# Kernel tuning notes

Measured on AMD Instinct MI355X. Metric: run time of the kernel, lower is better.

Reference implementation:

```python
import jax, jax.numpy as jnp
import numpy as np

GRID = 256  # hardcoded mask shape in the original module
SMOOTH = 1e-06
THRESH = 127.0


def _fill_polygon(pts):
    # pts: [N,1,2] in [0,1]; replicates the TF scan-line rasterizer, vectorized.
    p = jnp.clip(jnp.squeeze(pts, axis=1) * 255.0, 0.0, 255.0)  # [N,2]
    pj = jnp.roll(p, 1, axis=0)                                  # edge partner j=i-1 (wraps)
    y = jnp.arange(GRID, dtype=p.dtype)[:, None]                 # [R,1] scanline rows
    pi_y = p[None, :, 1]
    pj_y = pj[None, :, 1]
    # edge crosses scanline y (strict-below / at-or-above parity rule)
    cross = ((pi_y < y) & (pj_y >= y)) | ((pj_y < y) & (pi_y >= y))  # [R,N]
    denom = jnp.where(cross, pj_y - pi_y, 1.0)
    xint = p[None, :, 0] + (y - pi_y) / denom * (pj[None, :, 0] - p[None, :, 0])
    xs = jnp.sort(jnp.where(cross, xint, jnp.inf), axis=1)       # [R,N] valid xs first
    count = jnp.sum(cross, axis=1)                               # [R]
    starts = jnp.floor(xs[:, 0::2])                              # int cast of nonneg = floor
    ends = jnp.floor(xs[:, 1::2])                                # [R,P]
    pidx = jnp.arange(starts.shape[1])
    valid = (2 * pidx + 1)[None, :] < count[:, None]             # unpaired last node dropped
    xg = jnp.arange(GRID, dtype=p.dtype)
    span = ((xg[None, :, None] >= starts[:, None, :]) &
            (xg[None, :, None] <= ends[:, None, :]) &
            valid[:, None, :])                                   # [R,256,P]
    return jnp.any(span, axis=2).astype(jnp.float32)             # [256,256]


def _dice(y_true, y_pred):
    t = y_true.reshape(-1)
    q = y_pred.reshape(-1)
    inter = jnp.sum(t * q)
    return (2.0 * inter + SMOOTH) / (jnp.sum(t) + jnp.sum(q) + SMOOTH)


def setup_inputs() -> dict:
    key = jax.random.key(0)
    k1, k2 = jax.random.split(key)
    points = jax.random.uniform(k1, (64, 128, 1, 2), dtype=jnp.float32)
    dmap = jax.random.uniform(k2, (64, 256, 256, 1), dtype=jnp.float32)
    return {"points": points, "dmap": dmap}


def reference(points, dmap):
    masks = jax.vmap(_fill_polygon)(points)                       # [B,256,256]
    bin_mask = (dmap[..., 0] * 255.0 <= THRESH).astype(jnp.float32)  # [B,256,256]
    dices = jax.vmap(_dice)(masks, bin_mask)                      # [B]
    return jnp.mean(1.0 - dices)
```

## Files before the change

kernel.cpp:

```cpp
#include <hip/hip_runtime.h>

#define GRIDN  256
#define NPTS   128
#define NBATCH 64

__device__ __forceinline__ float2 scale_clip(float2 p) {
    return make_float2(fminf(fmaxf(p.x * 255.0f, 0.0f), 255.0f),
                       fminf(fmaxf(p.y * 255.0f, 0.0f), 255.0f));
}

__device__ __forceinline__ int covered(int A, int B) {
    const int hi = (A - 1) & ~1;
    const int lo = (B - 1) > 0 ? (B - 1) : 0;
    return (A > 0) && (hi >= lo);
}

__global__ __launch_bounds__(256) void fill_dice_kernel(
    const float* __restrict__ points,
    const float* __restrict__ dmap,
    unsigned int* __restrict__ acc)
{
#pragma clang fp contract(off)
    __shared__ unsigned int hist[4][GRIDN];
    __shared__ int psum[4][3];

    const int wave = threadIdx.x >> 6;
    const int lane = threadIdx.x & 63;
    const int blk  = blockIdx.x;
    const int b    = blk >> 6;
    const int y    = (blk & 63) * 4 + wave;
    const float yf = (float)y;

    *(uint4*)&hist[wave][lane * 4] = make_uint4(0u, 0u, 0u, 0u);

    const float* pb = points + b * NPTS * 2;

    const int j0 = 2 * lane;
    const int j1 = j0 + 1;
    const int jm = (j0 + NPTS - 1) & (NPTS - 1);

    const float2 Pm = scale_clip(*(const float2*)(pb + jm * 2));
    const float2 P0 = scale_clip(*(const float2*)(pb + j0 * 2));
    const float2 P1 = scale_clip(*(const float2*)(pb + j1 * 2));

    const bool c0 = (P0.y < yf && Pm.y >= yf) || (Pm.y < yf && P0.y >= yf);
    const bool c1 = (P1.y < yf && P0.y >= yf) || (P0.y < yf && P1.y >= yf);

    const float xi0 = P0.x + (yf - P0.y) / (Pm.y - P0.y) * (Pm.x - P0.x);
    const float xi1 = P1.x + (yf - P1.y) / (P0.y - P1.y) * (P0.x - P1.x);

    const int px = lane * 4;
    const float4 dv = *(const float4*)(dmap + (size_t)((b * GRIDN + y) * GRIDN + px));

    const int neg = __popcll(__ballot(c0 && xi0 < 0.0f))
                  + __popcll(__ballot(c1 && xi1 < 0.0f));

    __syncthreads();

    if (c0 && xi0 >= 0.0f) atomicAdd(&hist[wave][min((int)xi0, 255)], 1u);
    if (c1 && xi1 >= 0.0f) atomicAdd(&hist[wave][min((int)xi1, 255)], 1u);

    __syncthreads();

    const uint4 hv = *(const uint4*)&hist[wave][lane * 4];
    const int h0 = hv.x, h1 = hv.y, h2 = hv.z, h3 = hv.w;
    const int s = h0 + h1 + h2 + h3;
    int incl = s;
#pragma unroll
    for (int off = 1; off < 64; off <<= 1) {
        const int t = __shfl_up(incl, off);
        if (lane >= off) incl += t;
    }
    const int C0 = neg + incl - s;
    const int C1 = C0 + h0;
    const int C2 = C1 + h1;
    const int C3 = C2 + h2;
    const int C4 = C3 + h3;

    const int q0 = (dv.x * 255.0f <= 127.0f);
    const int q1 = (dv.y * 255.0f <= 127.0f);
    const int q2 = (dv.z * 255.0f <= 127.0f);
    const int q3 = (dv.w * 255.0f <= 127.0f);

    const int v0 = covered(C1, C0);
    const int v1 = covered(C2, C1);
    const int v2 = covered(C3, C2);
    const int v3 = covered(C4, C3);

    const int t_  = v0 + v1 + v2 + v3;
    const int it_ = v0 * q0 + v1 * q1 + v2 * q2 + v3 * q3;
    const int q_  = q0 + q1 + q2 + q3;

    int packed = it_ | (t_ << 10) | (q_ << 20);
#pragma unroll
    for (int off = 32; off; off >>= 1) packed += __shfl_xor(packed, off);

    if (lane == 0) {
        psum[wave][0] =  packed        & 1023;
        psum[wave][1] = (packed >> 10) & 1023;
        psum[wave][2] = (packed >> 20) & 1023;
    }
    __syncthreads();

    if (threadIdx.x < 3) {
        const int i = threadIdx.x;
        const int sum = psum[0][i] + psum[1][i] + psum[2][i] + psum[3][i];
        atomicAdd(&acc[b * 3 + i], (unsigned)sum);
    }
}

__global__ void finalize_kernel(const unsigned int* __restrict__ acc,
                                float* __restrict__ out)
{
    const int lane = threadIdx.x;
    const float I = (float)acc[lane * 3 + 0];
    const float T = (float)acc[lane * 3 + 1];
    const float Q = (float)acc[lane * 3 + 2];
    const float dice = (2.0f * I + 1e-6f) / (T + Q + 1e-6f);
    float loss = 1.0f - dice;
#pragma unroll
    for (int off = 32; off; off >>= 1) loss += __shfl_xor(loss, off);
    if (lane == 0) out[0] = loss * (1.0f / 64.0f);
}

extern "C" void kernel_launch(void* const* d_in, const int* in_sizes, int n_in,
                              void* d_out, int out_size, void* d_ws, size_t ws_size,
                              hipStream_t stream)
{
    const float* points = (const float*)d_in[0];
    const float* dmap   = (const float*)d_in[1];
    float* out          = (float*)d_out;
    unsigned int* acc   = (unsigned int*)d_ws;

    hipMemsetAsync(acc, 0, NBATCH * 3 * sizeof(unsigned int), stream);
    fill_dice_kernel<<<dim3(4096), dim3(256), 0, stream>>>(points, dmap, acc);
    finalize_kernel<<<dim3(1), dim3(64), 0, stream>>>(acc, out);
}
```

Baseline: 82.14 us.

## Process four scanlines per wave with byte-packed histograms and per-block partials

Each wave now handles four rows instead of one. The polygon point loads and edge setup are amortized across those rows, and the four row histograms are packed into bytes of one shared counter so a single prefix scan serves all four. Block syncs are replaced by explicit lgkmcnt waits. The coverage test is simplified to a parity-or-hit check, and global atomics plus the memset are replaced by per-block partial writes that the finalize kernel reduces. Launching four times fewer blocks cuts launch and per-block overhead and removes one memset launch, at the cost of less parallelism and of relying on no byte histogram bin exceeding 255.

```diff
diff --git a/kernel.cpp b/kernel.cpp
--- a/kernel.cpp
+++ b/kernel.cpp
@@ -3,124 +3,130 @@
 #define GRIDN  256
 #define NPTS   128
 #define NBATCH 64
+#define NBLK   1024
 
-__device__ __forceinline__ float2 scale_clip(float2 p) {
-    return make_float2(fminf(fmaxf(p.x * 255.0f, 0.0f), 255.0f),
-                       fminf(fmaxf(p.y * 255.0f, 0.0f), 255.0f));
-}
-
-__device__ __forceinline__ int covered(int A, int B) {
-    const int hi = (A - 1) & ~1;
-    const int lo = (B - 1) > 0 ? (B - 1) : 0;
-    return (A > 0) && (hi >= lo);
+__device__ __forceinline__ float clip255(float v) {
+    return fminf(fmaxf(v * 255.0f, 0.0f), 255.0f);
 }
 
 __global__ __launch_bounds__(256) void fill_dice_kernel(
     const float* __restrict__ points,
     const float* __restrict__ dmap,
-    unsigned int* __restrict__ acc)
+    uint4* __restrict__ partials)
 {
 #pragma clang fp contract(off)
     __shared__ unsigned int hist[4][GRIDN];
-    __shared__ int psum[4][3];
+    __shared__ unsigned long long psum[4];
 
-    const int wave = threadIdx.x >> 6;
-    const int lane = threadIdx.x & 63;
-    const int blk  = blockIdx.x;
-    const int b    = blk >> 6;
-    const int y    = (blk & 63) * 4 + wave;
-    const float yf = (float)y;
+    const int wave  = threadIdx.x >> 6;
+    const int lane  = threadIdx.x & 63;
+    const int blk   = blockIdx.x;
+    const int b     = blk >> 4;
+    const int ybase = (blk & 15) * 16 + wave * 4;
+
+    const float* drow = dmap + (size_t)(b * GRIDN + ybase) * GRIDN + lane * 4;
+    const float4 dv0 = *(const float4*)(drow);
+    const float4 dv1 = *(const float4*)(drow + GRIDN);
+    const float4 dv2 = *(const float4*)(drow + 2 * GRIDN);
+    const float4 dv3 = *(const float4*)(drow + 3 * GRIDN);
+
+    const float4 pv = *(const float4*)(points + b * NPTS * 2 + lane * 4);
+    const float p0x = clip255(pv.x), p0y = clip255(pv.y);
+    const float p1x = clip255(pv.z), p1y = clip255(pv.w);
+    const int   src = (lane + 63) & 63;
+    const float pmx = __shfl(p1x, src);
+    const float pmy = __shfl(p1y, src);
 
     *(uint4*)&hist[wave][lane * 4] = make_uint4(0u, 0u, 0u, 0u);
+    asm volatile("s_waitcnt lgkmcnt(0)" ::: "memory");
 
-    const float* pb = points + b * NPTS * 2;
+    const float d0y = pmy - p0y, d0x = pmx - p0x;
+    const float d1y = p0y - p1y, d1x = p0x - p1x;
 
-    const int j0 = 2 * lane;
-    const int j1 = j0 + 1;
-    const int jm = (j0 + NPTS - 1) & (NPTS - 1);
+    int neg0, neg1, neg2, neg3;
+#define CROSS_K(k, negk)                                                          \
+    {                                                                             \
+        const float yf = (float)(ybase + (k));                                    \
+        const bool c0 = (p0y < yf && pmy >= yf) || (pmy < yf && p0y >= yf);       \
+        const bool c1 = (p1y < yf && p0y >= yf) || (p0y < yf && p1y >= yf);       \
+        const float xi0 = p0x + (yf - p0y) / d0y * d0x;                           \
+        const float xi1 = p1x + (yf - p1y) / d1y * d1x;                           \
+        negk = __popcll(__ballot(c0 && xi0 < 0.0f))                               \
+             + __popcll(__ballot(c1 && xi1 < 0.0f));                              \
+        const unsigned int add = 1u << (8 * (k));                                 \
+        if (c0 && xi0 >= 0.0f) atomicAdd(&hist[wave][min((int)xi0, 255)], add);   \
+        if (c1 && xi1 >= 0.0f) atomicAdd(&hist[wave][min((int)xi1, 255)], add);   \
+    }
+    CROSS_K(0, neg0) CROSS_K(1, neg1) CROSS_K(2, neg2) CROSS_K(3, neg3)
+#undef CROSS_K
 
-    const float2 Pm = scale_clip(*(const float2*)(pb + jm * 2));
-    const float2 P0 = scale_clip(*(const float2*)(pb + j0 * 2));
-    const float2 P1 = scale_clip(*(const float2*)(pb + j1 * 2));
+    asm volatile("s_waitcnt lgkmcnt(0)" ::: "memory");
+    const uint4 hv = *(const uint4*)&hist[wave][lane * 4];
 
-    const bool c0 = (P0.y < yf && Pm.y >= yf) || (Pm.y < yf && P0.y >= yf);
-    const bool c1 = (P1.y < yf && P0.y >= yf) || (P0.y < yf && P1.y >= yf);
-
-    const float xi0 = P0.x + (yf - P0.y) / (Pm.y - P0.y) * (Pm.x - P0.x);
-    const float xi1 = P1.x + (yf - P1.y) / (P0.y - P1.y) * (P0.x - P1.x);
-
-    const int px = lane * 4;
-    const float4 dv = *(const float4*)(dmap + (size_t)((b * GRIDN + y) * GRIDN + px));
-
-    const int neg = __popcll(__ballot(c0 && xi0 < 0.0f))
-                  + __popcll(__ballot(c1 && xi1 < 0.0f));
-
-    __syncthreads();
-
-    if (c0 && xi0 >= 0.0f) atomicAdd(&hist[wave][min((int)xi0, 255)], 1u);
-    if (c1 && xi1 >= 0.0f) atomicAdd(&hist[wave][min((int)xi1, 255)], 1u);
-
-    __syncthreads();
-
-    const uint4 hv = *(const uint4*)&hist[wave][lane * 4];
-    const int h0 = hv.x, h1 = hv.y, h2 = hv.z, h3 = hv.w;
-    const int s = h0 + h1 + h2 + h3;
-    int incl = s;
+    const unsigned int s4 = hv.x + hv.y + hv.z + hv.w;
+    unsigned int incl = s4;
 #pragma unroll
     for (int off = 1; off < 64; off <<= 1) {
-        const int t = __shfl_up(incl, off);
+        const unsigned int t = __shfl_up(incl, off);
         if (lane >= off) incl += t;
     }
-    const int C0 = neg + incl - s;
-    const int C1 = C0 + h0;
-    const int C2 = C1 + h1;
-    const int C3 = C2 + h2;
-    const int C4 = C3 + h3;
+    const unsigned int excl = incl - s4;
 
-    const int q0 = (dv.x * 255.0f <= 127.0f);
-    const int q1 = (dv.y * 255.0f <= 127.0f);
-    const int q2 = (dv.z * 255.0f <= 127.0f);
-    const int q3 = (dv.w * 255.0f <= 127.0f);
+    int it_ = 0, t_ = 0, q_ = 0;
+#define PIX_K(k, negk, dvk)                                                       \
+    {                                                                             \
+        const int C0 = (int)((excl >> (8 * (k))) & 255u) + negk;                  \
+        const int h0 = (int)((hv.x >> (8 * (k))) & 255u);                         \
+        const int h1 = (int)((hv.y >> (8 * (k))) & 255u);                         \
+        const int h2 = (int)((hv.z >> (8 * (k))) & 255u);                         \
+        const int h3 = (int)((hv.w >> (8 * (k))) & 255u);                         \
+        const int C1 = C0 + h0, C2 = C1 + h1, C3 = C2 + h2;                       \
+        const int v0 = (C0 & 1) | (h0 != 0);                                      \
+        const int v1 = (C1 & 1) | (h1 != 0);                                      \
+        const int v2 = (C2 & 1) | (h2 != 0);                                      \
+        const int v3 = (C3 & 1) | (h3 != 0);                                      \
+        const int q0 = (dvk.x * 255.0f <= 127.0f);                                \
+        const int q1 = (dvk.y * 255.0f <= 127.0f);                                \
+        const int q2 = (dvk.z * 255.0f <= 127.0f);                                \
+        const int q3 = (dvk.w * 255.0f <= 127.0f);                                \
+        t_  += v0 + v1 + v2 + v3;                                                 \
+        q_  += q0 + q1 + q2 + q3;                                                 \
+        it_ += v0 * q0 + v1 * q1 + v2 * q2 + v3 * q3;                             \
+    }
+    PIX_K(0, neg0, dv0) PIX_K(1, neg1, dv1) PIX_K(2, neg2, dv2) PIX_K(3, neg3, dv3)
+#undef PIX_K
 
-    const int v0 = covered(C1, C0);
-    const int v1 = covered(C2, C1);
-    const int v2 = covered(C3, C2);
-    const int v3 = covered(C4, C3);
-
-    const int t_  = v0 + v1 + v2 + v3;
-    const int it_ = v0 * q0 + v1 * q1 + v2 * q2 + v3 * q3;
-    const int q_  = q0 + q1 + q2 + q3;
-
-    int packed = it_ | (t_ << 10) | (q_ << 20);
+    unsigned long long packed = (unsigned long long)it_
+                              | ((unsigned long long)t_ << 20)
+                              | ((unsigned long long)q_ << 40);
 #pragma unroll
     for (int off = 32; off; off >>= 1) packed += __shfl_xor(packed, off);
 
-    if (lane == 0) {
-        psum[wave][0] =  packed        & 1023;
-        psum[wave][1] = (packed >> 10) & 1023;
-        psum[wave][2] = (packed >> 20) & 1023;
-    }
+    if (lane == 0) psum[wave] = packed;
     __syncthreads();
-
-    if (threadIdx.x < 3) {
-        const int i = threadIdx.x;
-        const int sum = psum[0][i] + psum[1][i] + psum[2][i] + psum[3][i];
-        atomicAdd(&acc[b * 3 + i], (unsigned)sum);
+    if (threadIdx.x == 0) {
+        const unsigned long long tot = psum[0] + psum[1] + psum[2] + psum[3];
+        partials[blk] = make_uint4((unsigned)(tot & 0xFFFFFu),
+                                   (unsigned)((tot >> 20) & 0xFFFFFu),
+                                   (unsigned)((tot >> 40) & 0xFFFFFu), 0u);
     }
 }
 
-__global__ void finalize_kernel(const unsigned int* __restrict__ acc,
+__global__ void finalize_kernel(const uint4* __restrict__ partials,
                                 float* __restrict__ out)
 {
-    const int lane = threadIdx.x;
-    const float I = (float)acc[lane * 3 + 0];
-    const float T = (float)acc[lane * 3 + 1];
-    const float Q = (float)acc[lane * 3 + 2];
-    const float dice = (2.0f * I + 1e-6f) / (T + Q + 1e-6f);
+    const int b = threadIdx.x;
+    unsigned int I = 0, T = 0, Q = 0;
+#pragma unroll
+    for (int g = 0; g < 16; ++g) {
+        const uint4 p = partials[b * 16 + g];
+        I += p.x; T += p.y; Q += p.z;
+    }
+    const float dice = (2.0f * (float)I + 1e-6f) / ((float)T + (float)Q + 1e-6f);
     float loss = 1.0f - dice;
 #pragma unroll
     for (int off = 32; off; off >>= 1) loss += __shfl_xor(loss, off);
-    if (lane == 0) out[0] = loss * (1.0f / 64.0f);
+    if (b == 0) out[0] = loss * (1.0f / 64.0f);
 }
 
 extern "C" void kernel_launch(void* const* d_in, const int* in_sizes, int n_in,
@@ -130,9 +136,8 @@
     const float* points = (const float*)d_in[0];
     const float* dmap   = (const float*)d_in[1];
     float* out          = (float*)d_out;
-    unsigned int* acc   = (unsigned int*)d_ws;
+    uint4* partials     = (uint4*)d_ws;
 
-    hipMemsetAsync(acc, 0, NBATCH * 3 * sizeof(unsigned int), stream);
-    fill_dice_kernel<<<dim3(4096), dim3(256), 0, stream>>>(points, dmap, acc);
-    finalize_kernel<<<dim3(1), dim3(64), 0, stream>>>(acc, out);
+    fill_dice_kernel<<<dim3(NBLK), dim3(256), 0, stream>>>(points, dmap, partials);
+    finalize_kernel<<<dim3(1), dim3(64), 0, stream>>>(partials, out);
 }
```

Result: faster. 69.77 us (-15.1%).
